# Performance work log

Hardware: AMD Instinct MI355X
Metric: run time of the kernel (lower is better)

The kernel has to match this reference:

```python
import jax, jax.numpy as jnp
import numpy as np

SLOPE = 25.0  # snntorch fast_sigmoid default surrogate slope

@jax.custom_vjp
def spike(u):
    return (u > 0).astype(u.dtype)

def _spike_fwd(u):
    return spike(u), u

def _spike_bwd(u, g):
    return (g / (1.0 + SLOPE * jnp.abs(u)) ** 2,)

spike.defvjp(_spike_fwd, _spike_bwd)

def fake_quant(W):
    # brevitas-style int8 per-tensor symmetric fake-quant with STE
    s = jnp.max(jnp.abs(W)) / 127.0
    q = jnp.clip(jnp.round(W / s), -127.0, 127.0) * s
    return W + jax.lax.stop_gradient(q - W)

def setup_inputs() -> dict:
    key = jax.random.key(0)
    ks = jax.random.split(key, 8)
    B, NIN, T = 256, 512, 256
    H1, H2, OUT = 512, 512, 128
    data = jax.random.normal(ks[0], (B, NIN, T), dtype=jnp.float32)
    W1 = jax.random.normal(ks[1], (H1, NIN), dtype=jnp.float32) / np.sqrt(NIN)
    W2 = jax.random.normal(ks[2], (H2, H1), dtype=jnp.float32) / np.sqrt(H1)
    Wrec = jax.random.normal(ks[3], (H2, H2), dtype=jnp.float32) / np.sqrt(H2)
    W3 = jax.random.normal(ks[4], (OUT, H2), dtype=jnp.float32) / np.sqrt(H2)
    beta = jnp.float32(0.9)
    th = jnp.float32(1.0)
    return {"data": data, "W1": W1, "W2": W2, "Wrec": Wrec, "W3": W3,
            "beta1": beta, "th1": th, "beta_r": beta, "th_r": th,
            "beta2": beta, "th2": th}

def reference(data, W1, W2, Wrec, W3, beta1, th1, beta_r, th_r, beta2, th2):
    B = data.shape[0]
    H1, H2, OUT = W1.shape[0], W2.shape[0], W3.shape[0]
    W1q = fake_quant(W1)
    W2q = fake_quant(W2)
    Wrq = fake_quant(Wrec)
    W3q = fake_quant(W3)
    b1 = jnp.clip(beta1, 0.0, 1.0)
    br = jnp.clip(beta_r, 0.0, 1.0)
    b2 = jnp.clip(beta2, 0.0, 1.0)
    # time-major input: [T, B, NIN]
    xs = jnp.transpose(data, (2, 0, 1))

    def step(carry, x):
        m1, mr, sr, m2 = carry
        # leaky1: reset zero, reset_delay=False
        m1 = b1 * m1 + x @ W1q.T
        s1 = spike(m1 - th1)
        m1 = m1 * (1.0 - s1)
        # recurrent LIF (RLeaky-like), reset zero, reset_delay=True:
        # previous spike resets the membrane at the start of this step
        h = s1 @ W2q.T + sr @ Wrq.T
        mr = (br * mr + h) * (1.0 - sr)
        sr = spike(mr - th_r)
        # leaky2: reset zero, reset_delay=False
        m2 = b2 * m2 + sr @ W3q.T
        s2 = spike(m2 - th2)
        m2 = m2 * (1.0 - s2)
        return (m1, mr, sr, m2), s2

    init = (jnp.zeros((B, H1), jnp.float32),
            jnp.zeros((B, H2), jnp.float32),
            jnp.zeros((B, H2), jnp.float32),
            jnp.zeros((B, OUT), jnp.float32))
    _, spk_rec = jax.lax.scan(step, init, xs)
    return spk_rec  # [T, B, OUT]
```

## Files before the change

kernel.cpp:

```cpp
#include <hip/hip_runtime.h>

#define B_   256
#define NIN_ 512
#define T_   256
#define H1_  512
#define H2_  512
#define OUT_ 128

typedef __attribute__((ext_vector_type(8))) short bf16x8;
typedef __attribute__((ext_vector_type(4))) float f32x4;
typedef __attribute__((address_space(1))) const unsigned int* gl_cu;
typedef __attribute__((address_space(3))) unsigned int* ls_u;

__global__ void absmax_k(const float* __restrict__ W1, const float* __restrict__ W2,
                         const float* __restrict__ Wr, const float* __restrict__ W3,
                         float* __restrict__ scales) {
  const float* W; int n;
  switch (blockIdx.x) {
    case 0:  W = W1; n = H1_ * NIN_; break;
    case 1:  W = W2; n = H2_ * H1_;  break;
    case 2:  W = Wr; n = H2_ * H2_;  break;
    default: W = W3; n = OUT_ * H2_; break;
  }
  int tid = threadIdx.x;
  float m = 0.f;
  const float4* W4 = (const float4*)W;
  int n4 = n >> 2;
  for (int i = tid; i < n4; i += 256) {
    float4 v = W4[i];
    m = fmaxf(m, fmaxf(fmaxf(fabsf(v.x), fabsf(v.y)), fmaxf(fabsf(v.z), fabsf(v.w))));
  }
  __shared__ float red[256];
  red[tid] = m;
  __syncthreads();
  for (int s = 128; s > 0; s >>= 1) {
    if (tid < s) red[tid] = fmaxf(red[tid], red[tid + s]);
    __syncthreads();
  }
  if (tid == 0) scales[blockIdx.x] = red[0] / 127.0f;
}

__global__ void quant_all_k(const float* __restrict__ W1, const float* __restrict__ W2,
                            const float* __restrict__ Wr, const float* __restrict__ W3,
                            const float* __restrict__ scales,
                            float* __restrict__ W1qT, ushort* __restrict__ W2bf,
                            signed char* __restrict__ WrT, ushort* __restrict__ W3bf) {
  const int blk = blockIdx.x;
  if (blk < 1024) {
    int idx = blk * 256 + threadIdx.x;
    int h = idx & (H1_ - 1), i = idx >> 9;
    float s = scales[0];
    float q = rintf(W1[h * NIN_ + i] / s);
    q = fminf(fmaxf(q, -127.f), 127.f);
    W1qT[idx] = q * s;
  } else if (blk < 2048) {
    int idx = (blk - 1024) * 256 + threadIdx.x;
    float s = scales[1];
    float q = rintf(W2[idx] / s);
    q = fminf(fmaxf(q, -127.f), 127.f);
    W2bf[idx] = (ushort)(__float_as_uint(q) >> 16);
  } else if (blk < 3072) {
    int idx = (blk - 2048) * 256 + threadIdx.x;
    int r = idx >> 9, c = idx & (H2_ - 1);
    float s = scales[2];
    float q = rintf(Wr[idx] / s);
    q = fminf(fmaxf(q, -127.f), 127.f);
    WrT[(size_t)c * H2_ + r] = (signed char)q;
  } else {
    int idx = (blk - 3072) * 256 + threadIdx.x;
    float s = scales[3];
    float q = rintf(W3[idx] / s);
    q = fminf(fmaxf(q, -127.f), 127.f);
    W3bf[idx] = (ushort)(__float_as_uint(q) >> 16);
  }
}

__global__ __launch_bounds__(256) void gemm_cur1_k(const float* __restrict__ data,
                                                   const float* __restrict__ W1qT,
                                                   float* __restrict__ cur1) {
  const int b  = blockIdx.y;
  const int t0 = (blockIdx.x >> 2) << 7;
  const int h0 = (blockIdx.x & 3) << 7;
  const int tid = threadIdx.x;

  __shared__ float As[2][16][128];
  __shared__ float Bs[2][16][128];

  const int ty = tid >> 4, tx = tid & 15;
  const int wv = tid >> 6;
  const int ln = tid & 63;
  const int lrow = ln >> 5;
  const int lcol = ln & 31;

  float acc[8][8];
#pragma unroll
  for (int i = 0; i < 8; i++)
#pragma unroll
    for (int j = 0; j < 8; j++) acc[i][j] = 0.f;

  const float* dbase = data + (size_t)b * NIN_ * T_;

  auto issue = [&](int kb, int buf) {
#pragma unroll
    for (int j = 0; j < 2; j++) {
      const int kr = (wv << 2) + (j << 1);
      const float* ga = dbase + (size_t)(kb + kr + lrow) * T_ + t0 + (lcol << 2);
      __builtin_amdgcn_global_load_lds((gl_cu)ga, (ls_u)&As[buf][kr][0], 16, 0, 0);
      const float* gb = W1qT + (size_t)(kb + kr + lrow) * H1_ + h0 + (lcol << 2);
      __builtin_amdgcn_global_load_lds((gl_cu)gb, (ls_u)&Bs[buf][kr][0], 16, 0, 0);
    }
  };

  issue(0, 0);

  for (int p = 0; p < 32; p++) {
    const int cur = p & 1;
    __syncthreads();
    if (p < 31) issue((p + 1) << 4, cur ^ 1);
#pragma unroll
    for (int k = 0; k < 16; k++) {
      float4 A0 = *(const float4*)&As[cur][k][ty * 4];
      float4 A1 = *(const float4*)&As[cur][k][64 + ty * 4];
      float4 B0 = *(const float4*)&Bs[cur][k][tx * 4];
      float4 B1 = *(const float4*)&Bs[cur][k][64 + tx * 4];
      float a[8] = {A0.x, A0.y, A0.z, A0.w, A1.x, A1.y, A1.z, A1.w};
      float w[8] = {B0.x, B0.y, B0.z, B0.w, B1.x, B1.y, B1.z, B1.w};
#pragma unroll
      for (int i = 0; i < 8; i++)
#pragma unroll
        for (int j = 0; j < 8; j++)
          acc[i][j] = fmaf(a[i], w[j], acc[i][j]);
    }
  }

#pragma unroll
  for (int i = 0; i < 8; i++) {
    int row = (i < 4) ? (ty * 4 + i) : (64 + ty * 4 + (i - 4));
    float* op = cur1 + (size_t)(t0 + row) * (B_ * H1_) + (size_t)b * H1_ + h0;
    float4 cA = {acc[i][0], acc[i][1], acc[i][2], acc[i][3]};
    float4 cB = {acc[i][4], acc[i][5], acc[i][6], acc[i][7]};
    *(float4*)(op + tx * 4)      = cA;
    *(float4*)(op + 64 + tx * 4) = cB;
  }
}

__global__ __launch_bounds__(256) void scan1_k(const float* __restrict__ cur1,
                                               unsigned char* __restrict__ s1u,
                                               const float* __restrict__ beta1p,
                                               const float* __restrict__ th1p) {
  const int n = blockIdx.x * 256 + threadIdx.x;
  const float b1 = fminf(fmaxf(beta1p[0], 0.f), 1.f);
  const float th1 = th1p[0];
  const size_t S = (size_t)B_ * H1_;
  float m1 = 0.f;
  for (int t = 0; t < T_; t += 4) {
    float c0 = cur1[(size_t)t * S + n];
    float c1 = cur1[(size_t)(t + 1) * S + n];
    float c2 = cur1[(size_t)(t + 2) * S + n];
    float c3 = cur1[(size_t)(t + 3) * S + n];
    m1 = b1 * m1 + c0; bool s0 = m1 - th1 > 0.f; if (s0) m1 = 0.f;
    s1u[(size_t)t * S + n] = s0;
    m1 = b1 * m1 + c1; bool s1 = m1 - th1 > 0.f; if (s1) m1 = 0.f;
    s1u[(size_t)(t + 1) * S + n] = s1;
    m1 = b1 * m1 + c2; bool s2 = m1 - th1 > 0.f; if (s2) m1 = 0.f;
    s1u[(size_t)(t + 2) * S + n] = s2;
    m1 = b1 * m1 + c3; bool s3 = m1 - th1 > 0.f; if (s3) m1 = 0.f;
    s1u[(size_t)(t + 3) * S + n] = s3;
  }
}

__global__ __launch_bounds__(256) void gemm_spk_k(const unsigned char* __restrict__ A8,
                                                  const ushort* __restrict__ Bw,
                                                  float* __restrict__ C, int N) {
  __shared__ short As[128 * 72];
  __shared__ short Bs[128 * 72];
  const int tid = threadIdx.x;
  const int m0 = blockIdx.y << 7;
  const int n0 = blockIdx.x << 7;
  const int lane = tid & 63, wave = tid >> 6;
  const int quad = lane >> 4, lm = lane & 15;
  const int wm = wave << 5;

  f32x4 acc[2][8];
#pragma unroll
  for (int s = 0; s < 2; s++)
#pragma unroll
    for (int n = 0; n < 8; n++) acc[s][n] = (f32x4){0.f, 0.f, 0.f, 0.f};

  for (int kb = 0; kb < 512; kb += 64) {
    uint4 av[2], bv[4];
#pragma unroll
    for (int i = 0; i < 2; i++) {
      int ch = tid + (i << 8);
      int row = ch >> 2, offB = (ch & 3) << 4;
      av[i] = *(const uint4*)(A8 + (size_t)(m0 + row) * 512 + kb + offB);
    }
#pragma unroll
    for (int i = 0; i < 4; i++) {
      int ch = tid + (i << 8);
      int row = ch >> 3, off = (ch & 7) << 3;
      bv[i] = *(const uint4*)(Bw + (size_t)(n0 + row) * 512 + kb + off);
    }
    __syncthreads();
#pragma unroll
    for (int i = 0; i < 2; i++) {
      int ch = tid + (i << 8);
      int row = ch >> 2, offB = (ch & 3) << 4;
      unsigned u[4] = {av[i].x, av[i].y, av[i].z, av[i].w};
      unsigned d[8];
#pragma unroll
      for (int w = 0; w < 4; w++) {
        unsigned uu = u[w];
        d[2 * w]     = ((uu & 1u) | ((uu & 0x100u) << 8)) * 0x3F80u;
        d[2 * w + 1] = (((uu >> 16) & 1u) | ((uu & 0x1000000u) >> 8)) * 0x3F80u;
      }
      uint4* dst = (uint4*)&As[row * 72 + offB];
      dst[0] = make_uint4(d[0], d[1], d[2], d[3]);
      dst[1] = make_uint4(d[4], d[5], d[6], d[7]);
    }
#pragma unroll
    for (int i = 0; i < 4; i++) {
      int ch = tid + (i << 8);
      int row = ch >> 3, off = (ch & 7) << 3;
      *(uint4*)&Bs[row * 72 + off] = bv[i];
    }
    __syncthreads();
#pragma unroll
    for (int kc = 0; kc < 64; kc += 32) {
      bf16x8 af0 = *(const bf16x8*)&As[(wm + lm) * 72 + kc + quad * 8];
      bf16x8 af1 = *(const bf16x8*)&As[(wm + 16 + lm) * 72 + kc + quad * 8];
      bf16x8 bfr[8];
#pragma unroll
      for (int n = 0; n < 8; n++)
        bfr[n] = *(const bf16x8*)&Bs[((n << 4) + lm) * 72 + kc + quad * 8];
#pragma unroll
      for (int n = 0; n < 8; n++) {
        acc[0][n] = __builtin_amdgcn_mfma_f32_16x16x32_bf16(af0, bfr[n], acc[0][n], 0, 0, 0);
        acc[1][n] = __builtin_amdgcn_mfma_f32_16x16x32_bf16(af1, bfr[n], acc[1][n], 0, 0, 0);
      }
    }
    __syncthreads();
  }

#pragma unroll
  for (int s = 0; s < 2; s++)
#pragma unroll
    for (int n = 0; n < 8; n++) {
      int row = m0 + wm + (s << 4) + quad * 4;
      int col = n0 + (n << 4) + lm;
#pragma unroll
      for (int r = 0; r < 4; r++)
        C[(size_t)(row + r) * N + col] = acc[s][n][r];
    }
}

__device__ __forceinline__ void unp_add(unsigned w, int* a) {
  int iw = (int)w;
  a[0] += (iw << 24) >> 24;
  a[1] += (iw << 16) >> 24;
  a[2] += (iw << 8) >> 24;
  a[3] += iw >> 24;
}

__global__ __launch_bounds__(1024) void recurrent_k(
    const float* __restrict__ cur2a,
    const signed char* __restrict__ WrT,
    unsigned char* __restrict__ sru,
    const float* __restrict__ scales,
    const float* __restrict__ betarp, const float* __restrict__ thrp) {
  const int b = blockIdx.x;
  const int tid = threadIdx.x;
  const float s2sc = scales[1];
  const float srsc = scales[2];
  const float br = fminf(fmaxf(betarp[0], 0.f), 1.f);
  const float thr = thrp[0];

  const unsigned* WrT4 = (const unsigned*)WrT;

  __shared__ unsigned WrL[256 * 128];
  __shared__ int red[8][H2_];
  __shared__ int lstLo[2][256];
  __shared__ int lstHi[2][256];
  __shared__ int ncLo[2], ncHi[2];

  {
    const uint4* src = (const uint4*)WrT4;
    uint4* dst = (uint4*)WrL;
    for (int i = tid; i < 8192; i += 1024) dst[i] = src[i];
  }
  if (tid < 2) { ncLo[tid] = 0; ncHi[tid] = 0; }
  __syncthreads();

  float mr = 0.f, sr_own = 0.f;
  const int g = tid >> 7;
  const int c = tid & 127;

  for (int t = 0; t < T_; t++) {
    const int old = t & 1, nxt = old ^ 1;
    float c2 = 0.f;
    if (tid < H2_) c2 = cur2a[((size_t)t * B_ + b) * H2_ + tid];
    if (tid == 1022) ncLo[nxt] = 0;
    if (tid == 1023) ncHi[nxt] = 0;
    const int nLo = ncLo[old];
    const int nHi = ncHi[old];
    const int* LLo = lstLo[old];
    const int* LHi = lstHi[old];

    int a4[4] = {0, 0, 0, 0};
    {
      int k = g;
      for (; k + 56 < nLo; k += 64) {
        int i0 = LLo[k],      i1 = LLo[k + 8],  i2 = LLo[k + 16], i3 = LLo[k + 24];
        int i4 = LLo[k + 32], i5 = LLo[k + 40], i6 = LLo[k + 48], i7 = LLo[k + 56];
        unsigned w0 = WrL[(i0 << 7) + c], w1 = WrL[(i1 << 7) + c];
        unsigned w2 = WrL[(i2 << 7) + c], w3 = WrL[(i3 << 7) + c];
        unsigned w4 = WrL[(i4 << 7) + c], w5 = WrL[(i5 << 7) + c];
        unsigned w6 = WrL[(i6 << 7) + c], w7 = WrL[(i7 << 7) + c];
        unp_add(w0, a4); unp_add(w1, a4); unp_add(w2, a4); unp_add(w3, a4);
        unp_add(w4, a4); unp_add(w5, a4); unp_add(w6, a4); unp_add(w7, a4);
      }
      for (; k + 24 < nLo; k += 32) {
        int i0 = LLo[k], i1 = LLo[k + 8], i2 = LLo[k + 16], i3 = LLo[k + 24];
        unsigned w0 = WrL[(i0 << 7) + c], w1 = WrL[(i1 << 7) + c];
        unsigned w2 = WrL[(i2 << 7) + c], w3 = WrL[(i3 << 7) + c];
        unp_add(w0, a4); unp_add(w1, a4); unp_add(w2, a4); unp_add(w3, a4);
      }
      for (; k < nLo; k += 8) unp_add(WrL[(LLo[k] << 7) + c], a4);
    }
    {
      int k = g;
      for (; k + 56 < nHi; k += 64) {
        int i0 = LHi[k],      i1 = LHi[k + 8],  i2 = LHi[k + 16], i3 = LHi[k + 24];
        int i4 = LHi[k + 32], i5 = LHi[k + 40], i6 = LHi[k + 48], i7 = LHi[k + 56];
        unsigned w0 = WrT4[(i0 << 7) + c], w1 = WrT4[(i1 << 7) + c];
        unsigned w2 = WrT4[(i2 << 7) + c], w3 = WrT4[(i3 << 7) + c];
        unsigned w4 = WrT4[(i4 << 7) + c], w5 = WrT4[(i5 << 7) + c];
        unsigned w6 = WrT4[(i6 << 7) + c], w7 = WrT4[(i7 << 7) + c];
        unp_add(w0, a4); unp_add(w1, a4); unp_add(w2, a4); unp_add(w3, a4);
        unp_add(w4, a4); unp_add(w5, a4); unp_add(w6, a4); unp_add(w7, a4);
      }
      for (; k + 24 < nHi; k += 32) {
        int i0 = LHi[k], i1 = LHi[k + 8], i2 = LHi[k + 16], i3 = LHi[k + 24];
        unsigned w0 = WrT4[(i0 << 7) + c], w1 = WrT4[(i1 << 7) + c];
        unsigned w2 = WrT4[(i2 << 7) + c], w3 = WrT4[(i3 << 7) + c];
        unp_add(w0, a4); unp_add(w1, a4); unp_add(w2, a4); unp_add(w3, a4);
      }
      for (; k < nHi; k += 8) unp_add(WrT4[(LHi[k] << 7) + c], a4);
    }
    *(int4*)&red[g][c << 2] = make_int4(a4[0], a4[1], a4[2], a4[3]);
    __syncthreads();

    bool spike = false;
    if (tid < H2_) {
      int acc = red[0][tid] + red[1][tid] + red[2][tid] + red[3][tid]
              + red[4][tid] + red[5][tid] + red[6][tid] + red[7][tid];
      float h = s2sc * c2 + srsc * (float)acc;
      mr = (br * mr + h) * (1.f - sr_own);
      sr_own = (mr - thr > 0.f) ? 1.f : 0.f;
      sru[((size_t)t * B_ + b) * H2_ + tid] = (unsigned char)(sr_own != 0.f);
      spike = (sr_own != 0.f);
    }
    unsigned long long bm = __ballot(spike);
    if (bm != 0ull) {
      const int lane = tid & 63;
      const int ldr = (int)__ffsll((long long)bm) - 1;
      int* cnt = (tid < 256) ? &ncLo[nxt] : &ncHi[nxt];
      int* dst = (tid < 256) ? lstLo[nxt] : lstHi[nxt];
      int base = 0;
      if (lane == ldr) base = atomicAdd(cnt, (int)__popcll(bm));
      base = __shfl(base, ldr);
      if (spike)
        dst[base + (int)__popcll(bm & ((1ull << lane) - 1ull))] = tid;
    }
    __syncthreads();
  }
}

__global__ __launch_bounds__(256) void scan3_k(const float* __restrict__ cur3,
                                               float* __restrict__ out,
                                               const float* __restrict__ scales,
                                               const float* __restrict__ beta2p,
                                               const float* __restrict__ th2p) {
  const int n = blockIdx.x * 256 + threadIdx.x;
  const float s3sc = scales[3];
  const float b2 = fminf(fmaxf(beta2p[0], 0.f), 1.f);
  const float th2 = th2p[0];
  const size_t S = (size_t)B_ * OUT_;
  float m2 = 0.f;
  for (int t = 0; t < T_; t += 4) {
    float v0 = cur3[(size_t)t * S + n];
    float v1 = cur3[(size_t)(t + 1) * S + n];
    float v2 = cur3[(size_t)(t + 2) * S + n];
    float v3 = cur3[(size_t)(t + 3) * S + n];
    m2 = b2 * m2 + s3sc * v0; float p0 = (m2 - th2 > 0.f) ? 1.f : 0.f; m2 *= (1.f - p0);
    out[(size_t)t * S + n] = p0;
    m2 = b2 * m2 + s3sc * v1; float p1 = (m2 - th2 > 0.f) ? 1.f : 0.f; m2 *= (1.f - p1);
    out[(size_t)(t + 1) * S + n] = p1;
    m2 = b2 * m2 + s3sc * v2; float p2 = (m2 - th2 > 0.f) ? 1.f : 0.f; m2 *= (1.f - p2);
    out[(size_t)(t + 2) * S + n] = p2;
    m2 = b2 * m2 + s3sc * v3; float p3 = (m2 - th2 > 0.f) ? 1.f : 0.f; m2 *= (1.f - p3);
    out[(size_t)(t + 3) * S + n] = p3;
  }
}

extern "C" void kernel_launch(void* const* d_in, const int* in_sizes, int n_in,
                              void* d_out, int out_size, void* d_ws, size_t ws_size,
                              hipStream_t stream) {
  const float* data  = (const float*)d_in[0];
  const float* W1    = (const float*)d_in[1];
  const float* W2    = (const float*)d_in[2];
  const float* Wr    = (const float*)d_in[3];
  const float* W3    = (const float*)d_in[4];
  const float* beta1 = (const float*)d_in[5];
  const float* th1   = (const float*)d_in[6];
  const float* betar = (const float*)d_in[7];
  const float* thr   = (const float*)d_in[8];
  const float* beta2 = (const float*)d_in[9];
  const float* th2   = (const float*)d_in[10];

  char* ws = (char*)d_ws;
  float*         scales = (float*)ws;
  float*         W1qT   = (float*)(ws + 4096);
  ushort*        W2bf   = (ushort*)(ws + 4096 + 1048576);
  ushort*        W3bf   = (ushort*)(ws + 4096 + 1048576 + 524288);
  signed char*   WrT    = (signed char*)(ws + 4096 + 1048576 + 524288 + 131072);
  float*         regA   = (float*)(ws + (size_t)4194304);
  unsigned char* regB   = (unsigned char*)(ws + (size_t)4194304 + 134217728);

  float* cur1  = regA;
  float* cur2a = regA;
  float* cur3  = regA;
  unsigned char* s1u = regB;
  unsigned char* sru = regB + (size_t)33554432;

  hipLaunchKernelGGL(absmax_k, dim3(4), dim3(256), 0, stream, W1, W2, Wr, W3, scales);
  hipLaunchKernelGGL(quant_all_k, dim3(3328), dim3(256), 0, stream,
                     W1, W2, Wr, W3, scales, W1qT, W2bf, WrT, W3bf);

  hipLaunchKernelGGL(gemm_cur1_k, dim3(8, 256), dim3(256), 0, stream, data, W1qT, cur1);
  hipLaunchKernelGGL(scan1_k, dim3((B_ * H1_) / 256), dim3(256), 0, stream, cur1, s1u, beta1, th1);
  hipLaunchKernelGGL(gemm_spk_k, dim3(4, 512), dim3(256), 0, stream, s1u, W2bf, cur2a, H2_);
  hipLaunchKernelGGL(recurrent_k, dim3(256), dim3(1024), 0, stream, cur2a, WrT, sru, scales, betar, thr);
  hipLaunchKernelGGL(gemm_spk_k, dim3(1, 512), dim3(256), 0, stream, sru, W3bf, cur3, OUT_);
  hipLaunchKernelGGL(scan3_k, dim3((B_ * OUT_) / 256), dim3(256), 0, stream, cur3, (float*)d_out, scales, beta2, th2);
}
```

Measured before the change: 1.030 ms.

## Parallelize absmax with atomics, deepen cur1 GEMM K tile, pack int8 accumulation

The weight absmax reduction now runs on 64 blocks per tensor and merges partial maxima with an atomicMax on the float bit pattern, replacing one block per tensor. An init kernel zeroes the slots first. The fp32 cur1 GEMM stages 32 K rows per step instead of 16, which halves the number of barrier iterations but doubles LDS use per block. In the recurrent kernel, the int8 weight unpacking is replaced by SWAR accumulation: each word is biased by XOR 0x80808080 and even and odd bytes are summed into 16-bit lanes, with the bias subtracted at the end. This cuts the ALU work per spike gathered, and the 16-bit lanes cannot overflow at these list lengths.

Measured after the change: 1.156 ms. 1.12x slower.

```diff
diff --git a/kernel.cpp b/kernel.cpp
--- a/kernel.cpp
+++ b/kernel.cpp
@@ -12,21 +12,26 @@
 typedef __attribute__((address_space(1))) const unsigned int* gl_cu;
 typedef __attribute__((address_space(3))) unsigned int* ls_u;
 
+__global__ void init_k(unsigned* __restrict__ bits) {
+  if (threadIdx.x < 4) bits[threadIdx.x] = 0u;
+}
+
 __global__ void absmax_k(const float* __restrict__ W1, const float* __restrict__ W2,
                          const float* __restrict__ Wr, const float* __restrict__ W3,
-                         float* __restrict__ scales) {
-  const float* W; int n;
-  switch (blockIdx.x) {
-    case 0:  W = W1; n = H1_ * NIN_; break;
-    case 1:  W = W2; n = H2_ * H1_;  break;
-    case 2:  W = Wr; n = H2_ * H2_;  break;
-    default: W = W3; n = OUT_ * H2_; break;
-  }
-  int tid = threadIdx.x;
+                         unsigned* __restrict__ bits) {
+  const int tensor = blockIdx.x >> 6;
+  const int chunk  = blockIdx.x & 63;
+  const float* W; int n4;
+  switch (tensor) {
+    case 0:  W = W1; n4 = (H1_ * NIN_) >> 2; break;
+    case 1:  W = W2; n4 = (H2_ * H1_) >> 2;  break;
+    case 2:  W = Wr; n4 = (H2_ * H2_) >> 2;  break;
+    default: W = W3; n4 = (OUT_ * H2_) >> 2; break;
+  }
+  const int tid = threadIdx.x;
   float m = 0.f;
   const float4* W4 = (const float4*)W;
-  int n4 = n >> 2;
-  for (int i = tid; i < n4; i += 256) {
+  for (int i = chunk * 256 + tid; i < n4; i += 64 * 256) {
     float4 v = W4[i];
     m = fmaxf(m, fmaxf(fmaxf(fabsf(v.x), fabsf(v.y)), fmaxf(fabsf(v.z), fabsf(v.w))));
   }
@@ -37,38 +42,40 @@
     if (tid < s) red[tid] = fmaxf(red[tid], red[tid + s]);
     __syncthreads();
   }
-  if (tid == 0) scales[blockIdx.x] = red[0] / 127.0f;
+  if (tid == 0) atomicMax(&bits[tensor], __float_as_uint(red[0]));
 }
 
 __global__ void quant_all_k(const float* __restrict__ W1, const float* __restrict__ W2,
                             const float* __restrict__ Wr, const float* __restrict__ W3,
-                            const float* __restrict__ scales,
+                            const unsigned* __restrict__ bits, float* __restrict__ scales,
                             float* __restrict__ W1qT, ushort* __restrict__ W2bf,
                             signed char* __restrict__ WrT, ushort* __restrict__ W3bf) {
   const int blk = blockIdx.x;
+  if (blk == 0 && threadIdx.x < 4)
+    scales[threadIdx.x] = __uint_as_float(bits[threadIdx.x]) / 127.0f;
   if (blk < 1024) {
     int idx = blk * 256 + threadIdx.x;
     int h = idx & (H1_ - 1), i = idx >> 9;
-    float s = scales[0];
+    float s = __uint_as_float(bits[0]) / 127.0f;
     float q = rintf(W1[h * NIN_ + i] / s);
     q = fminf(fmaxf(q, -127.f), 127.f);
     W1qT[idx] = q * s;
   } else if (blk < 2048) {
     int idx = (blk - 1024) * 256 + threadIdx.x;
-    float s = scales[1];
+    float s = __uint_as_float(bits[1]) / 127.0f;
     float q = rintf(W2[idx] / s);
     q = fminf(fmaxf(q, -127.f), 127.f);
     W2bf[idx] = (ushort)(__float_as_uint(q) >> 16);
   } else if (blk < 3072) {
     int idx = (blk - 2048) * 256 + threadIdx.x;
     int r = idx >> 9, c = idx & (H2_ - 1);
-    float s = scales[2];
+    float s = __uint_as_float(bits[2]) / 127.0f;
     float q = rintf(Wr[idx] / s);
     q = fminf(fmaxf(q, -127.f), 127.f);
     WrT[(size_t)c * H2_ + r] = (signed char)q;
   } else {
     int idx = (blk - 3072) * 256 + threadIdx.x;
-    float s = scales[3];
+    float s = __uint_as_float(bits[3]) / 127.0f;
     float q = rintf(W3[idx] / s);
     q = fminf(fmaxf(q, -127.f), 127.f);
     W3bf[idx] = (ushort)(__float_as_uint(q) >> 16);
@@ -83,8 +90,8 @@
   const int h0 = (blockIdx.x & 3) << 7;
   const int tid = threadIdx.x;
 
-  __shared__ float As[2][16][128];
-  __shared__ float Bs[2][16][128];
+  __shared__ float As[2][32][128];
+  __shared__ float Bs[2][32][128];
 
   const int ty = tid >> 4, tx = tid & 15;
   const int wv = tid >> 6;
@@ -102,8 +109,8 @@
 
   auto issue = [&](int kb, int buf) {
 #pragma unroll
-    for (int j = 0; j < 2; j++) {
-      const int kr = (wv << 2) + (j << 1);
+    for (int j = 0; j < 4; j++) {
+      const int kr = (wv << 3) + (j << 1);
       const float* ga = dbase + (size_t)(kb + kr + lrow) * T_ + t0 + (lcol << 2);
       __builtin_amdgcn_global_load_lds((gl_cu)ga, (ls_u)&As[buf][kr][0], 16, 0, 0);
       const float* gb = W1qT + (size_t)(kb + kr + lrow) * H1_ + h0 + (lcol << 2);
@@ -113,12 +120,12 @@
 
   issue(0, 0);
 
-  for (int p = 0; p < 32; p++) {
+  for (int p = 0; p < 16; p++) {
     const int cur = p & 1;
     __syncthreads();
-    if (p < 31) issue((p + 1) << 4, cur ^ 1);
-#pragma unroll
-    for (int k = 0; k < 16; k++) {
+    if (p < 15) issue((p + 1) << 5, cur ^ 1);
+#pragma unroll
+    for (int k = 0; k < 32; k++) {
       float4 A0 = *(const float4*)&As[cur][k][ty * 4];
       float4 A1 = *(const float4*)&As[cur][k][64 + ty * 4];
       float4 B0 = *(const float4*)&Bs[cur][k][tx * 4];
@@ -254,13 +261,7 @@
     }
 }
 
-__device__ __forceinline__ void unp_add(unsigned w, int* a) {
-  int iw = (int)w;
-  a[0] += (iw << 24) >> 24;
-  a[1] += (iw << 16) >> 24;
-  a[2] += (iw << 8) >> 24;
-  a[3] += iw >> 24;
-}
+#define PACC(w) { unsigned x_ = (w) ^ 0x80808080u; aE += x_ & 0x00FF00FFu; aO += (x_ >> 8) & 0x00FF00FFu; }
 
 __global__ __launch_bounds__(1024) void recurrent_k(
     const float* __restrict__ cur2a,
@@ -308,6 +309,8 @@
 
     int a4[4] = {0, 0, 0, 0};
     {
+      unsigned aE = 0, aO = 0;
+      const int cnt = (nLo > g) ? ((nLo - g + 7) >> 3) : 0;
       int k = g;
       for (; k + 56 < nLo; k += 64) {
         int i0 = LLo[k],      i1 = LLo[k + 8],  i2 = LLo[k + 16], i3 = LLo[k + 24];
@@ -316,18 +319,18 @@
         unsigned w2 = WrL[(i2 << 7) + c], w3 = WrL[(i3 << 7) + c];
         unsigned w4 = WrL[(i4 << 7) + c], w5 = WrL[(i5 << 7) + c];
         unsigned w6 = WrL[(i6 << 7) + c], w7 = WrL[(i7 << 7) + c];
-        unp_add(w0, a4); unp_add(w1, a4); unp_add(w2, a4); unp_add(w3, a4);
-        unp_add(w4, a4); unp_add(w5, a4); unp_add(w6, a4); unp_add(w7, a4);
+        PACC(w0) PACC(w1) PACC(w2) PACC(w3) PACC(w4) PACC(w5) PACC(w6) PACC(w7)
       }
-      for (; k + 24 < nLo; k += 32) {
-        int i0 = LLo[k], i1 = LLo[k + 8], i2 = LLo[k + 16], i3 = LLo[k + 24];
-        unsigned w0 = WrL[(i0 << 7) + c], w1 = WrL[(i1 << 7) + c];
-        unsigned w2 = WrL[(i2 << 7) + c], w3 = WrL[(i3 << 7) + c];
-        unp_add(w0, a4); unp_add(w1, a4); unp_add(w2, a4); unp_add(w3, a4);
-      }
-      for (; k < nLo; k += 8) unp_add(WrL[(LLo[k] << 7) + c], a4);
+      for (; k < nLo; k += 8) PACC(WrL[(LLo[k] << 7) + c])
+      const int bias = cnt << 7;
+      a4[0] += (int)(aE & 0xFFFFu) - bias;
+      a4[1] += (int)(aO & 0xFFFFu) - bias;
+      a4[2] += (int)(aE >> 16) - bias;
+      a4[3] += (int)(aO >> 16) - bias;
     }
     {
+      unsigned aE = 0, aO = 0;
+      const int cnt = (nHi > g) ? ((nHi - g + 7) >> 3) : 0;
       int k = g;
       for (; k + 56 < nHi; k += 64) {
         int i0 = LHi[k],      i1 = LHi[k + 8],  i2 = LHi[k + 16], i3 = LHi[k + 24];
@@ -336,16 +339,14 @@
         unsigned w2 = WrT4[(i2 << 7) + c], w3 = WrT4[(i3 << 7) + c];
         unsigned w4 = WrT4[(i4 << 7) + c], w5 = WrT4[(i5 << 7) + c];
         unsigned w6 = WrT4[(i6 << 7) + c], w7 = WrT4[(i7 << 7) + c];
-        unp_add(w0, a4); unp_add(w1, a4); unp_add(w2, a4); unp_add(w3, a4);
-        unp_add(w4, a4); unp_add(w5, a4); unp_add(w6, a4); unp_add(w7, a4);
+        PACC(w0) PACC(w1) PACC(w2) PACC(w3) PACC(w4) PACC(w5) PACC(w6) PACC(w7)
       }
-      for (; k + 24 < nHi; k += 32) {
-        int i0 = LHi[k], i1 = LHi[k + 8], i2 = LHi[k + 16], i3 = LHi[k + 24];
-        unsigned w0 = WrT4[(i0 << 7) + c], w1 = WrT4[(i1 << 7) + c];
-        unsigned w2 = WrT4[(i2 << 7) + c], w3 = WrT4[(i3 << 7) + c];
-        unp_add(w0, a4); unp_add(w1, a4); unp_add(w2, a4); unp_add(w3, a4);
-      }
-      for (; k < nHi; k += 8) unp_add(WrT4[(LHi[k] << 7) + c], a4);
+      for (; k < nHi; k += 8) PACC(WrT4[(LHi[k] << 7) + c])
+      const int bias = cnt << 7;
+      a4[0] += (int)(aE & 0xFFFFu) - bias;
+      a4[1] += (int)(aO & 0xFFFFu) - bias;
+      a4[2] += (int)(aE >> 16) - bias;
+      a4[3] += (int)(aO >> 16) - bias;
     }
     *(int4*)&red[g][c << 2] = make_int4(a4[0], a4[1], a4[2], a4[3]);
     __syncthreads();
@@ -420,6 +421,7 @@
 
   char* ws = (char*)d_ws;
   float*         scales = (float*)ws;
+  unsigned*      bits   = (unsigned*)(ws + 256);
   float*         W1qT   = (float*)(ws + 4096);
   ushort*        W2bf   = (ushort*)(ws + 4096 + 1048576);
   ushort*        W3bf   = (ushort*)(ws + 4096 + 1048576 + 524288);
@@ -433,9 +435,10 @@
   unsigned char* s1u = regB;
   unsigned char* sru = regB + (size_t)33554432;
 
-  hipLaunchKernelGGL(absmax_k, dim3(4), dim3(256), 0, stream, W1, W2, Wr, W3, scales);
+  hipLaunchKernelGGL(init_k, dim3(1), dim3(64), 0, stream, bits);
+  hipLaunchKernelGGL(absmax_k, dim3(256), dim3(256), 0, stream, W1, W2, Wr, W3, bits);
   hipLaunchKernelGGL(quant_all_k, dim3(3328), dim3(256), 0, stream,
-                     W1, W2, Wr, W3, scales, W1qT, W2bf, WrT, W3bf);
+                     W1, W2, Wr, W3, bits, scales, W1qT, W2bf, WrT, W3bf);
 
   hipLaunchKernelGGL(gemm_cur1_k, dim3(8, 256), dim3(256), 0, stream, data, W1qT, cur1);
   hipLaunchKernelGGL(scan1_k, dim3((B_ * H1_) / 256), dim3(256), 0, stream, cur1, s1u, beta1, th1);
```
